# Kernel optimization log

Hardware: AMD Instinct MI355X
Metric: run time of the kernel (lower is better)

Reference implementation:

```python
import jax, jax.numpy as jnp
import numpy as np

DIM = 96
D_STATE = 16
D_CONV = 3
D_INNER = 192   # int(DIM * 2.0)
DT_RANK = 6     # ceil(DIM / 16)
K = 4           # cross-scan directions
BATCH, H, W = 2, 56, 56


def setup_inputs() -> dict:
    key = jax.random.key(0)
    k = jax.random.split(key, 8)
    x = jax.random.normal(k[0], (BATCH, DIM, H, W), jnp.float32)
    W_in = jax.random.normal(k[1], (DIM, 2 * D_INNER), jnp.float32) / np.sqrt(DIM)
    W_conv = jax.random.normal(k[2], (D_INNER, 1, D_CONV, D_CONV), jnp.float32) / D_CONV
    b_conv = jnp.zeros((D_INNER,), jnp.float32)
    W_xproj = jax.random.normal(k[3], (K, D_INNER, DT_RANK + 2 * D_STATE), jnp.float32) / np.sqrt(D_INNER)
    W_dt = jax.random.normal(k[4], (K, DT_RANK, D_INNER), jnp.float32) / np.sqrt(DT_RANK)
    # dt bias init as in torch: dt ~ exp(U * (log 0.1 - log 0.001) + log 0.001), inv-softplus
    dt = jnp.exp(jax.random.uniform(k[5], (K, D_INNER), jnp.float32)
                 * (np.log(0.1) - np.log(0.001)) + np.log(0.001))
    dt = jnp.clip(dt, 1e-4, None)
    b_dt = dt + jnp.log(-jnp.expm1(-dt))
    A_logs = jnp.log(jnp.broadcast_to(jnp.arange(1, D_STATE + 1, dtype=jnp.float32),
                                      (K, D_INNER, D_STATE)))
    Ds = jnp.ones((K, D_INNER), jnp.float32)
    W_out = jax.random.normal(k[6], (D_INNER, DIM), jnp.float32) / np.sqrt(D_INNER)
    return dict(x=x, W_in=W_in, W_conv=W_conv, b_conv=b_conv, W_xproj=W_xproj,
                W_dt=W_dt, b_dt=b_dt, A_logs=A_logs, Ds=Ds, W_out=W_out)


def _ss2d(x, W_in, W_conv, b_conv, W_xproj, W_dt, b_dt, A_logs, Ds, W_out):
    Bsz, C, Hh, Ww = x.shape
    L = Hh * Ww
    # in_proj
    xf = x.transpose(0, 2, 3, 1).reshape(Bsz, L, C)        # (B, L, C)
    xz = xf @ W_in
    xp, z = jnp.split(xz, 2, axis=-1)                       # each (B, L, D)
    # depthwise conv + silu
    xi = xp.reshape(Bsz, Hh, Ww, -1).transpose(0, 3, 1, 2)  # (B, D, H, W)
    pad = D_CONV // 2
    xi = jax.lax.conv_general_dilated(
        xi, W_conv, (1, 1), ((pad, pad), (pad, pad)),
        feature_group_count=xi.shape[1],
        dimension_numbers=('NCHW', 'OIHW', 'NCHW')) + b_conv[None, :, None, None]
    xi = jax.nn.silu(xi)
    D = xi.shape[1]
    # cross-scan: 4 directions, each (B, L, D)
    x1 = xi.reshape(Bsz, D, L).transpose(0, 2, 1)
    x2 = xi[:, :, :, ::-1].reshape(Bsz, D, L).transpose(0, 2, 1)
    xt = xi.transpose(0, 1, 3, 2)                           # (B, D, W, H)
    x3 = xt.reshape(Bsz, D, L).transpose(0, 2, 1)
    x4 = xt[:, :, :, ::-1].reshape(Bsz, D, L).transpose(0, 2, 1)
    xs = jnp.stack([x1, x2, x3, x4])                        # (K, B, L, D)
    # per-direction projections, batched over K
    xdbl = jnp.einsum('kbld,kde->kble', xs, W_xproj)
    dr = xdbl[..., :DT_RANK]
    Bk = xdbl[..., DT_RANK:DT_RANK + D_STATE]               # (K, B, L, N)
    Ck = xdbl[..., DT_RANK + D_STATE:]                      # (K, B, L, N)
    delta = jax.nn.softplus(jnp.einsum('kblr,krd->kbld', dr, W_dt)
                            + b_dt[:, None, None, :])       # (K, B, L, D)
    A = -jnp.exp(A_logs)                                    # (K, D, N)

    def step(h, inp):
        x_i, d_i, B_i, C_i = inp  # (K,B,D), (K,B,D), (K,B,N), (K,B,N)
        dA = jnp.exp(d_i[..., None] * A[:, None])           # (K, B, D, N)
        h = dA * h + (d_i * x_i)[..., None] * B_i[:, :, None, :]
        y = jnp.einsum('kbdn,kbn->kbd', h, C_i)
        return h, y

    h0 = jnp.zeros((K, Bsz, D, D_STATE), xs.dtype)
    seq = (xs.transpose(2, 0, 1, 3), delta.transpose(2, 0, 1, 3),
           Bk.transpose(2, 0, 1, 3), Ck.transpose(2, 0, 1, 3))
    _, ys = jax.lax.scan(step, h0, seq)                     # (L, K, B, D)
    ys = ys.transpose(1, 2, 0, 3) + xs * Ds[:, None, None, :]  # (K, B, L, D)
    # cross-merge back to row-major (h w) order
    y1 = ys[0]
    y2 = ys[1].reshape(Bsz, Hh, Ww, D)[:, :, ::-1, :].reshape(Bsz, L, D)
    y3 = ys[2].reshape(Bsz, Ww, Hh, D).transpose(0, 2, 1, 3).reshape(Bsz, L, D)
    y4 = ys[3].reshape(Bsz, Ww, Hh, D)[:, :, ::-1, :].transpose(0, 2, 1, 3).reshape(Bsz, L, D)
    y = (y1 + y2 + y3 + y4) * jax.nn.silu(z)
    out = (y @ W_out).reshape(Bsz, Hh, Ww, C).transpose(0, 3, 1, 2)
    return out


def reference(x, W_in, W_conv, b_conv, W_xproj, W_dt, b_dt, A_logs, Ds, W_out):
    return _ss2d(x, W_in, W_conv, b_conv, W_xproj, W_dt, b_dt, A_logs, Ds, W_out)
```

## Files before the change

kernel.cpp:

```cpp
#include <hip/hip_runtime.h>
#include <math.h>

constexpr int BATCH  = 2;
constexpr int CDIM   = 96;
constexpr int HH     = 56;
constexpr int WW     = 56;
constexpr int LL     = HH * WW;
constexpr int DIN    = 192;
constexpr int NK     = 4;
constexpr int NST    = 16;
constexpr int RNK    = 6;
constexpr int EPROJ  = RNK + 2 * NST;
constexpr int SCH    = 64;
constexpr int NCH    = LL / SCH;
constexpr int CGRP   = DIN / 16;

constexpr int STDU = SCH + 2;
constexpr int STBC = SCH + 6;
constexpr int STY  = SCH + 4;
constexpr int STB1 = SCH + 4;

constexpr size_t SZ_PX   = (size_t)BATCH * LL * DIN;
constexpr size_t OFF_XP  = 0;
constexpr size_t OFF_Z   = OFF_XP + SZ_PX;
constexpr size_t OFF_XI  = OFF_Z  + SZ_PX;
constexpr size_t OFF_DR  = OFF_XI + SZ_PX;
constexpr size_t SZ_DR   = (size_t)NK * BATCH * LL * 8;
constexpr size_t OFF_B   = OFF_DR + SZ_DR;
constexpr size_t SZ_BC   = (size_t)NK * BATCH * LL * NST;
constexpr size_t OFF_C   = OFF_B + SZ_BC;
constexpr size_t OFF_YD  = OFF_C + SZ_BC;
constexpr size_t SZ_YD   = (size_t)NK * BATCH * LL * DIN;
constexpr size_t OFF_HE  = OFF_YD + SZ_YD;
constexpr size_t SZ_HS   = (size_t)NK * BATCH * NCH * DIN * NST;
constexpr size_t OFF_HI  = OFF_HE + SZ_HS;
constexpr size_t OFF_WT  = OFF_HI + SZ_HS;
constexpr size_t SZ_WT   = (size_t)NK * EPROJ * DIN;

__device__ __forceinline__ float silu(float v) {
    return v / (1.0f + __expf(-v));
}

__device__ __forceinline__ float softplus_f(float x) {
    return (x > 20.0f) ? x : __logf(1.0f + __expf(x));
}

__device__ __forceinline__ float row_reduce16(float p) {
    p += __int_as_float(__builtin_amdgcn_update_dpp(0, __float_as_int(p), 0x128, 0xf, 0xf, true));
    p += __int_as_float(__builtin_amdgcn_update_dpp(0, __float_as_int(p), 0x124, 0xf, 0xf, true));
    p += __int_as_float(__builtin_amdgcn_update_dpp(0, __float_as_int(p), 0x122, 0xf, 0xf, true));
    p += __int_as_float(__builtin_amdgcn_update_dpp(0, __float_as_int(p), 0x121, 0xf, 0xf, true));
    return p;
}

__device__ __forceinline__ int seq_to_lr(int k, int l) {
    int q = l / WW;
    int r = l - q * WW;
    if (k == 0) return l;
    if (k == 1) return q * WW + (WW - 1 - r);
    if (k == 2) return r * WW + q;
    return (WW - 1 - r) * WW + q;
}

__device__ __forceinline__ int spatial_to_seq(int k, int s) {
    int h = s / WW;
    int w = s - h * WW;
    if (k == 0) return s;
    if (k == 1) return h * WW + (WW - 1 - w);
    if (k == 2) return w * WW + h;
    return w * WW + (WW - 1 - h);
}

__device__ __forceinline__ size_t hs_idx(int c, int kb, int d, int n) {
    return ((size_t)(c * (NK * BATCH) + kb) * DIN + d) * NST + n;
}

__device__ __forceinline__ float4 delta4(
        float4 r03, float2 r45, const float4* wr, float4 bb4) {
    float4 raw = bb4;
    raw.x = fmaf(r03.x, wr[0].x, raw.x); raw.y = fmaf(r03.x, wr[0].y, raw.y);
    raw.z = fmaf(r03.x, wr[0].z, raw.z); raw.w = fmaf(r03.x, wr[0].w, raw.w);
    raw.x = fmaf(r03.y, wr[1].x, raw.x); raw.y = fmaf(r03.y, wr[1].y, raw.y);
    raw.z = fmaf(r03.y, wr[1].z, raw.z); raw.w = fmaf(r03.y, wr[1].w, raw.w);
    raw.x = fmaf(r03.z, wr[2].x, raw.x); raw.y = fmaf(r03.z, wr[2].y, raw.y);
    raw.z = fmaf(r03.z, wr[2].z, raw.z); raw.w = fmaf(r03.z, wr[2].w, raw.w);
    raw.x = fmaf(r03.w, wr[3].x, raw.x); raw.y = fmaf(r03.w, wr[3].y, raw.y);
    raw.z = fmaf(r03.w, wr[3].z, raw.z); raw.w = fmaf(r03.w, wr[3].w, raw.w);
    raw.x = fmaf(r45.x, wr[4].x, raw.x); raw.y = fmaf(r45.x, wr[4].y, raw.y);
    raw.z = fmaf(r45.x, wr[4].z, raw.z); raw.w = fmaf(r45.x, wr[4].w, raw.w);
    raw.x = fmaf(r45.y, wr[5].x, raw.x); raw.y = fmaf(r45.y, wr[5].y, raw.y);
    raw.z = fmaf(r45.y, wr[5].z, raw.z); raw.w = fmaf(r45.y, wr[5].w, raw.w);
    raw.x = softplus_f(raw.x); raw.y = softplus_f(raw.y);
    raw.z = softplus_f(raw.z); raw.w = softplus_f(raw.w);
    return raw;
}

constexpr int K1_PIX = 8;
__global__ __launch_bounds__(384) void k_inproj(
        const float* __restrict__ x, const float* __restrict__ W_in,
        const float* __restrict__ W_xproj,
        float* __restrict__ xp, float* __restrict__ z, float* __restrict__ Wt) {
    __shared__ float sxT[CDIM][K1_PIX];
    int gp0 = blockIdx.x * K1_PIX;
    int t   = threadIdx.x;
    int b   = gp0 / LL;
    int l0  = gp0 - b * LL;
    int gid = blockIdx.x * 384 + t;
    if (gid < NK * DIN * EPROJ) {
        int k = gid / (DIN * EPROJ);
        int r = gid % (DIN * EPROJ);
        int d = r / EPROJ;
        int e = r % EPROJ;
        Wt[((size_t)k * EPROJ + e) * DIN + d] = W_xproj[gid];
    }
    for (int i = t; i < CDIM * K1_PIX; i += 384) {
        int c = i >> 3, p = i & 7;
        sxT[c][p] = x[((size_t)(b * CDIM + c)) * LL + l0 + p];
    }
    __syncthreads();
    int e = t;
    float acc[K1_PIX];
#pragma unroll
    for (int p = 0; p < K1_PIX; p++) acc[p] = 0.0f;
    const float4* sx4 = (const float4*)sxT;
#pragma unroll 4
    for (int c = 0; c < CDIM; c++) {
        float w  = W_in[c * (2 * DIN) + e];
        float4 va = sx4[2 * c];
        float4 vb = sx4[2 * c + 1];
        acc[0] = fmaf(va.x, w, acc[0]); acc[1] = fmaf(va.y, w, acc[1]);
        acc[2] = fmaf(va.z, w, acc[2]); acc[3] = fmaf(va.w, w, acc[3]);
        acc[4] = fmaf(vb.x, w, acc[4]); acc[5] = fmaf(vb.y, w, acc[5]);
        acc[6] = fmaf(vb.z, w, acc[6]); acc[7] = fmaf(vb.w, w, acc[7]);
    }
    if (e < DIN) {
#pragma unroll
        for (int p = 0; p < K1_PIX; p++)
            xp[((size_t)(gp0 + p)) * DIN + e] = acc[p];
    } else {
        int e2 = e - DIN;
#pragma unroll
        for (int p = 0; p < K1_PIX; p++)
            z[((size_t)(gp0 + p)) * DIN + e2] = acc[p];
    }
}

__global__ __launch_bounds__(192) void k_conv(
        const float* __restrict__ xp, const float* __restrict__ Wc,
        const float* __restrict__ bc, float* __restrict__ xi) {
    int gp = blockIdx.x;
    int d  = threadIdx.x;
    int b  = gp / LL;
    int l  = gp - b * LL;
    int h  = l / WW;
    int w  = l - h * WW;
    float acc = bc[d];
#pragma unroll
    for (int dy = -1; dy <= 1; dy++) {
        int hh = h + dy;
        if (hh < 0 || hh >= HH) continue;
#pragma unroll
        for (int dx = -1; dx <= 1; dx++) {
            int ww = w + dx;
            if (ww < 0 || ww >= WW) continue;
            acc = fmaf(xp[((size_t)b * LL + hh * WW + ww) * DIN + d],
                       Wc[d * 9 + (dy + 1) * 3 + (dx + 1)], acc);
        }
    }
    xi[(size_t)gp * DIN + d] = silu(acc);
}

constexpr int K3_PIX = 32;
__global__ __launch_bounds__(256) void k_xproj(
        const float* __restrict__ xi, const float* __restrict__ Wt,
        float* __restrict__ drbuf, float* __restrict__ Bbuf,
        float* __restrict__ Cbuf) {
    __shared__ float4 v4[K3_PIX][49];
    __shared__ float4 sw4[EPROJ][49];
    int k   = blockIdx.y;
    int gp0 = blockIdx.x * K3_PIX;
    int b   = gp0 / LL;
    int l0  = gp0 - b * LL;
    int t   = threadIdx.x;
    const float4* xin4 = (const float4*)(xi + (size_t)gp0 * DIN);
    for (int i = t; i < K3_PIX * 48; i += 256)
        v4[i / 48][i % 48] = xin4[i];
    const float4* wt4 = (const float4*)(Wt + (size_t)k * EPROJ * DIN);
    for (int i = t; i < EPROJ * 48; i += 256)
        sw4[i / 48][i % 48] = wt4[i];
    __syncthreads();
    int p0 = t & 15;
    int eg = t >> 4;
    bool has3 = (eg < EPROJ - 32);
    float acc[2][3] = {{0.f, 0.f, 0.f}, {0.f, 0.f, 0.f}};
    for (int j = 0; j < 48; j++) {
        float4 w0 = sw4[eg][j];
        float4 w1 = sw4[eg + 16][j];
        float4 w2 = has3 ? sw4[eg + 32][j] : make_float4(0.f, 0.f, 0.f, 0.f);
#pragma unroll
        for (int q = 0; q < 2; q++) {
            float4 vv = v4[p0 + 16 * q][j];
            acc[q][0] = fmaf(vv.x, w0.x, acc[q][0]); acc[q][0] = fmaf(vv.y, w0.y, acc[q][0]);
            acc[q][0] = fmaf(vv.z, w0.z, acc[q][0]); acc[q][0] = fmaf(vv.w, w0.w, acc[q][0]);
            acc[q][1] = fmaf(vv.x, w1.x, acc[q][1]); acc[q][1] = fmaf(vv.y, w1.y, acc[q][1]);
            acc[q][1] = fmaf(vv.z, w1.z, acc[q][1]); acc[q][1] = fmaf(vv.w, w1.w, acc[q][1]);
            acc[q][2] = fmaf(vv.x, w2.x, acc[q][2]); acc[q][2] = fmaf(vv.y, w2.y, acc[q][2]);
            acc[q][2] = fmaf(vv.z, w2.z, acc[q][2]); acc[q][2] = fmaf(vv.w, w2.w, acc[q][2]);
        }
    }
#pragma unroll
    for (int q = 0; q < 2; q++) {
        int p  = p0 + 16 * q;
        int ls = spatial_to_seq(k, l0 + p);
        size_t kb  = (size_t)(k * BATCH + b);
        size_t b8  = (kb * LL + ls) * 8;
        size_t b16 = (kb * LL + ls) * NST;
        if (eg < RNK) drbuf[b8 + eg] = acc[q][0];
        else          Bbuf[b16 + eg - RNK] = acc[q][0];
        int e1 = eg + 16;
        if (e1 < RNK + NST) Bbuf[b16 + e1 - RNK] = acc[q][1];
        else                Cbuf[b16 + e1 - RNK - NST] = acc[q][1];
        if (has3) Cbuf[b16 + eg + 32 - RNK - NST] = acc[q][2];
    }
}

__global__ __launch_bounds__(256) void k_scanA(
        const float* __restrict__ xi, const float* __restrict__ drbuf,
        const float* __restrict__ Bbuf, const float* __restrict__ A_logs,
        const float* __restrict__ W_dt, const float* __restrict__ b_dt,
        float* __restrict__ Pbuf, float* __restrict__ hend) {
    __shared__ float2 sDU2[16][STDU];
    __shared__ float  sB1t[16][STB1];
    int c   = blockIdx.x;
    int blk = blockIdx.y;
    int k   = blk / (BATCH * CGRP);
    int rem = blk % (BATCH * CGRP);
    int b   = rem / CGRP;
    int cg  = rem % CGRP;
    int d0  = cg * 16;
    int t    = threadIdx.x;
    int lane = t & 63, wave = t >> 6;
    int grp  = lane >> 4, n = lane & 15;
    int ch   = wave * 4 + grp;
    int d    = d0 + ch;
    float A = -__expf(A_logs[((size_t)(k * DIN + d)) * NST + n]);
    size_t kb = (size_t)(k * BATCH + b);
    const float* drp = drbuf + kb * LL * 8;
    const float* bp  = Bbuf  + kb * LL * NST;
    const float* up  = xi    + (size_t)b * LL * DIN;
    int ss  = t >> 2;
    int cc0 = (t & 3) * 4;
    float4 wr[RNK];
#pragma unroll
    for (int r = 0; r < RNK; r++)
        wr[r] = *(const float4*)(W_dt + ((size_t)k * RNK + r) * DIN + d0 + cc0);
    float4 bb4 = *(const float4*)(b_dt + k * DIN + d0 + cc0);
    int l0 = c * SCH;
    {
        int l  = l0 + ss;
        int lr = seq_to_lr(k, l);
        float4 r03 = *(const float4*)(drp + (size_t)l * 8);
        float2 r45 = *(const float2*)(drp + (size_t)l * 8 + 4);
        float4 dlt = delta4(r03, r45, wr, bb4);
        float4 u4  = *(const float4*)(up + (size_t)lr * DIN + d0 + cc0);
        float4 B4  = *(const float4*)(bp + (size_t)l * NST + cc0);
        sDU2[cc0 + 0][ss] = make_float2(dlt.x, dlt.x * u4.x);
        sDU2[cc0 + 1][ss] = make_float2(dlt.y, dlt.y * u4.y);
        sDU2[cc0 + 2][ss] = make_float2(dlt.z, dlt.z * u4.z);
        sDU2[cc0 + 3][ss] = make_float2(dlt.w, dlt.w * u4.w);
        sB1t[cc0 + 0][ss] = B4.x;
        sB1t[cc0 + 1][ss] = B4.y;
        sB1t[cc0 + 2][ss] = B4.z;
        sB1t[cc0 + 3][ss] = B4.w;
    }
    __syncthreads();
    float h = 0.0f, P = 1.0f;
#pragma unroll 2
    for (int s4 = 0; s4 < SCH; s4 += 4) {
        float4 duA = *(const float4*)&sDU2[ch][s4];
        float4 duB = *(const float4*)&sDU2[ch][s4 + 2];
        float4 bq  = *(const float4*)&sB1t[n][s4];
        float dA;
        dA = __expf(duA.x * A); h = fmaf(dA, h, duA.y * bq.x); P *= dA;
        dA = __expf(duA.z * A); h = fmaf(dA, h, duA.w * bq.y); P *= dA;
        dA = __expf(duB.x * A); h = fmaf(dA, h, duB.y * bq.z); P *= dA;
        dA = __expf(duB.z * A); h = fmaf(dA, h, duB.w * bq.w); P *= dA;
    }
    size_t idx = hs_idx(c, (int)kb, d, n);
    Pbuf[idx] = P;
    hend[idx] = h;
}

__global__ __launch_bounds__(256) void k_scanB(
        const float* __restrict__ Pbuf, const float* __restrict__ hend,
        float* __restrict__ hin) {
    int tid = blockIdx.x * 256 + threadIdx.x;
    int kb  = tid / (DIN * NST);
    int dn  = tid % (DIN * NST);
    float h = 0.0f;
    for (int c = 0; c < NCH; c++) {
        size_t idx = ((size_t)(c * (NK * BATCH) + kb)) * (DIN * NST) + dn;
        hin[idx] = h;
        h = fmaf(Pbuf[idx], h, hend[idx]);
    }
}

__global__ __launch_bounds__(256) void k_scanC(
        const float* __restrict__ xi, const float* __restrict__ drbuf,
        const float* __restrict__ Bbuf, const float* __restrict__ Cbuf,
        const float* __restrict__ A_logs, const float* __restrict__ W_dt,
        const float* __restrict__ b_dt, const float* __restrict__ hin,
        float* __restrict__ ydir) {
    __shared__ float2 sDU2[16][STDU];
    __shared__ float2 sBC2[16][STBC];
    __shared__ float  sY[16][STY];
    int c   = blockIdx.x;
    int blk = blockIdx.y;
    int k   = blk / (BATCH * CGRP);
    int rem = blk % (BATCH * CGRP);
    int b   = rem / CGRP;
    int cg  = rem % CGRP;
    int d0  = cg * 16;
    int t    = threadIdx.x;
    int lane = t & 63, wave = t >> 6;
    int grp  = lane >> 4, n = lane & 15;
    int ch   = wave * 4 + grp;
    int d    = d0 + ch;
    float A = -__expf(A_logs[((size_t)(k * DIN + d)) * NST + n]);
    size_t kb = (size_t)(k * BATCH + b);
    const float* drp = drbuf + kb * LL * 8;
    const float* bp  = Bbuf  + kb * LL * NST;
    const float* cp  = Cbuf  + kb * LL * NST;
    const float* up  = xi    + (size_t)b * LL * DIN;
    float*       yp  = ydir  + kb * LL * DIN;
    int ss  = t >> 2;
    int cc0 = (t & 3) * 4;
    float4 wr[RNK];
#pragma unroll
    for (int r = 0; r < RNK; r++)
        wr[r] = *(const float4*)(W_dt + ((size_t)k * RNK + r) * DIN + d0 + cc0);
    float4 bb4 = *(const float4*)(b_dt + k * DIN + d0 + cc0);
    int l0 = c * SCH;
    {
        int l  = l0 + ss;
        int lr = seq_to_lr(k, l);
        float4 r03 = *(const float4*)(drp + (size_t)l * 8);
        float2 r45 = *(const float2*)(drp + (size_t)l * 8 + 4);
        float4 dlt = delta4(r03, r45, wr, bb4);
        float4 u4  = *(const float4*)(up + (size_t)lr * DIN + d0 + cc0);
        float4 B4  = *(const float4*)(bp + (size_t)l * NST + cc0);
        float4 C4  = *(const float4*)(cp + (size_t)l * NST + cc0);
        sDU2[cc0 + 0][ss] = make_float2(dlt.x, dlt.x * u4.x);
        sDU2[cc0 + 1][ss] = make_float2(dlt.y, dlt.y * u4.y);
        sDU2[cc0 + 2][ss] = make_float2(dlt.z, dlt.z * u4.z);
        sDU2[cc0 + 3][ss] = make_float2(dlt.w, dlt.w * u4.w);
        sBC2[cc0 + 0][ss] = make_float2(B4.x, C4.x);
        sBC2[cc0 + 1][ss] = make_float2(B4.y, C4.y);
        sBC2[cc0 + 2][ss] = make_float2(B4.z, C4.z);
        sBC2[cc0 + 3][ss] = make_float2(B4.w, C4.w);
    }
    float h = hin[hs_idx(c, (int)kb, d, n)];
    __syncthreads();
#pragma unroll 2
    for (int s4 = 0; s4 < SCH; s4 += 4) {
        float4 duA = *(const float4*)&sDU2[ch][s4];
        float4 duB = *(const float4*)&sDU2[ch][s4 + 2];
        float4 bcA = *(const float4*)&sBC2[n][s4];
        float4 bcB = *(const float4*)&sBC2[n][s4 + 2];
        float dA, y0, y1, y2, y3;
        dA = __expf(duA.x * A); h = fmaf(dA, h, duA.y * bcA.x); y0 = row_reduce16(h * bcA.y);
        dA = __expf(duA.z * A); h = fmaf(dA, h, duA.w * bcA.z); y1 = row_reduce16(h * bcA.w);
        dA = __expf(duB.x * A); h = fmaf(dA, h, duB.y * bcB.x); y2 = row_reduce16(h * bcB.y);
        dA = __expf(duB.z * A); h = fmaf(dA, h, duB.w * bcB.z); y3 = row_reduce16(h * bcB.w);
        if (n == 0) *(float4*)&sY[ch][s4] = make_float4(y0, y1, y2, y3);
    }
    __syncthreads();
    for (int i = t; i < SCH * 16; i += 256) {
        int s = i >> 4, cc = i & 15;
        int lr = seq_to_lr(k, l0 + s);
        yp[(size_t)lr * DIN + d0 + cc] = sY[cc][s];
    }
}

constexpr int K5_PIX = 8;
__global__ __launch_bounds__(192) void k_out(
        const float* __restrict__ ydir, const float* __restrict__ xi,
        const float* __restrict__ zbuf, const float* __restrict__ Ds,
        const float* __restrict__ W_out, float* __restrict__ out) {
    __shared__ float g[DIN][12];
    __shared__ float so[CDIM][9];
    int gp0 = blockIdx.x * K5_PIX;
    int b   = gp0 / LL;
    int l0  = gp0 - b * LL;
    int t   = threadIdx.x;
    for (int i = t; i < K5_PIX * DIN; i += 192) {
        int p = i / DIN, dd = i % DIN;
        size_t off = (size_t)(gp0 + p) * DIN + dd;
        float y = ydir[off] + ydir[SZ_PX + off]
                + ydir[2 * SZ_PX + off] + ydir[3 * SZ_PX + off];
        float dsum = Ds[dd] + Ds[DIN + dd] + Ds[2 * DIN + dd] + Ds[3 * DIN + dd];
        y = fmaf(xi[off], dsum, y);
        g[dd][p] = y * silu(zbuf[off]);
    }
    __syncthreads();
    int f    = t % CDIM;
    int half = t / CDIM;
    float acc[4] = {0.f, 0.f, 0.f, 0.f};
#pragma unroll 4
    for (int dd = 0; dd < DIN; dd++) {
        float wv = W_out[dd * CDIM + f];
        float4 gv = *(const float4*)&g[dd][half * 4];
        acc[0] = fmaf(gv.x, wv, acc[0]);
        acc[1] = fmaf(gv.y, wv, acc[1]);
        acc[2] = fmaf(gv.z, wv, acc[2]);
        acc[3] = fmaf(gv.w, wv, acc[3]);
    }
#pragma unroll
    for (int p = 0; p < 4; p++) so[f][half * 4 + p] = acc[p];
    __syncthreads();
    for (int i = t; i < CDIM * K5_PIX; i += 192) {
        int f2 = i / K5_PIX, p2 = i % K5_PIX;
        out[((size_t)(b * CDIM + f2)) * LL + l0 + p2] = so[f2][p2];
    }
}

extern "C" void kernel_launch(void* const* d_in, const int* in_sizes, int n_in,
                              void* d_out, int out_size, void* d_ws, size_t ws_size,
                              hipStream_t stream) {
    const float* x       = (const float*)d_in[0];
    const float* W_in    = (const float*)d_in[1];
    const float* W_conv  = (const float*)d_in[2];
    const float* b_conv  = (const float*)d_in[3];
    const float* W_xproj = (const float*)d_in[4];
    const float* W_dt    = (const float*)d_in[5];
    const float* b_dt    = (const float*)d_in[6];
    const float* A_logs  = (const float*)d_in[7];
    const float* Ds      = (const float*)d_in[8];
    const float* W_out   = (const float*)d_in[9];
    float* out = (float*)d_out;
    float* ws  = (float*)d_ws;

    float* xp    = ws + OFF_XP;
    float* z     = ws + OFF_Z;
    float* xi    = ws + OFF_XI;
    float* drbuf = ws + OFF_DR;
    float* Bbuf  = ws + OFF_B;
    float* Cbuf  = ws + OFF_C;
    float* ydir  = ws + OFF_YD;
    float* hend  = ws + OFF_HE;
    float* hin   = ws + OFF_HI;
    float* Wt    = ws + OFF_WT;
    float* Pbuf  = xp;

    k_inproj<<<(BATCH * LL) / K1_PIX, 384, 0, stream>>>(x, W_in, W_xproj, xp, z, Wt);
    k_conv<<<BATCH * LL, DIN, 0, stream>>>(xp, W_conv, b_conv, xi);
    dim3 g3((BATCH * LL) / K3_PIX, NK);
    k_xproj<<<g3, 256, 0, stream>>>(xi, Wt, drbuf, Bbuf, Cbuf);
    dim3 gs(NCH, NK * BATCH * CGRP);
    k_scanA<<<gs, 256, 0, stream>>>(xi, drbuf, Bbuf, A_logs, W_dt, b_dt, Pbuf, hend);
    k_scanB<<<(NK * BATCH * DIN * NST) / 256, 256, 0, stream>>>(Pbuf, hend, hin);
    k_scanC<<<gs, 256, 0, stream>>>(xi, drbuf, Bbuf, Cbuf, A_logs, W_dt, b_dt, hin, ydir);
    k_out<<<(BATCH * LL) / K5_PIX, 192, 0, stream>>>(ydir, xi, z, Ds, W_out, out);
}
```

Measured before the change: 207.6 us.

## Materialize transposed xi copy so column-major scan directions read contiguously

The conv kernel now also writes a width-major (transposed) copy of the activated input. Directions 2 and 3 read this copy in the x-projection and scan kernels, so their per-sequence-step input loads become row-contiguous instead of strided by a full image row. Their outputs stay in transposed order and are un-transposed in the output kernel's gather. This trades an extra strided store in conv and extra workspace for coalesced reads in the scan passes.

```diff
diff --git a/kernel.cpp b/kernel.cpp
--- a/kernel.cpp
+++ b/kernel.cpp
@@ -24,7 +24,8 @@
 constexpr size_t OFF_XP  = 0;
 constexpr size_t OFF_Z   = OFF_XP + SZ_PX;
 constexpr size_t OFF_XI  = OFF_Z  + SZ_PX;
-constexpr size_t OFF_DR  = OFF_XI + SZ_PX;
+constexpr size_t OFF_XIT = OFF_XI + SZ_PX;
+constexpr size_t OFF_DR  = OFF_XIT + SZ_PX;
 constexpr size_t SZ_DR   = (size_t)NK * BATCH * LL * 8;
 constexpr size_t OFF_B   = OFF_DR + SZ_DR;
 constexpr size_t SZ_BC   = (size_t)NK * BATCH * LL * NST;
@@ -35,7 +36,6 @@
 constexpr size_t SZ_HS   = (size_t)NK * BATCH * NCH * DIN * NST;
 constexpr size_t OFF_HI  = OFF_HE + SZ_HS;
 constexpr size_t OFF_WT  = OFF_HI + SZ_HS;
-constexpr size_t SZ_WT   = (size_t)NK * EPROJ * DIN;
 
 __device__ __forceinline__ float silu(float v) {
     return v / (1.0f + __expf(-v));
@@ -43,6 +43,11 @@
 
 __device__ __forceinline__ float softplus_f(float x) {
     return (x > 20.0f) ? x : __logf(1.0f + __expf(x));
+}
+
+__device__ __forceinline__ int rev56(int l) {
+    int r = l % WW;
+    return l + 55 - 2 * r;
 }
 
 __device__ __forceinline__ float row_reduce16(float p) {
@@ -51,24 +56,6 @@
     p += __int_as_float(__builtin_amdgcn_update_dpp(0, __float_as_int(p), 0x122, 0xf, 0xf, true));
     p += __int_as_float(__builtin_amdgcn_update_dpp(0, __float_as_int(p), 0x121, 0xf, 0xf, true));
     return p;
-}
-
-__device__ __forceinline__ int seq_to_lr(int k, int l) {
-    int q = l / WW;
-    int r = l - q * WW;
-    if (k == 0) return l;
-    if (k == 1) return q * WW + (WW - 1 - r);
-    if (k == 2) return r * WW + q;
-    return (WW - 1 - r) * WW + q;
-}
-
-__device__ __forceinline__ int spatial_to_seq(int k, int s) {
-    int h = s / WW;
-    int w = s - h * WW;
-    if (k == 0) return s;
-    if (k == 1) return h * WW + (WW - 1 - w);
-    if (k == 2) return w * WW + h;
-    return w * WW + (WW - 1 - h);
 }
 
 __device__ __forceinline__ size_t hs_idx(int c, int kb, int d, int n) {
@@ -147,7 +134,8 @@
 
 __global__ __launch_bounds__(192) void k_conv(
         const float* __restrict__ xp, const float* __restrict__ Wc,
-        const float* __restrict__ bc, float* __restrict__ xi) {
+        const float* __restrict__ bc, float* __restrict__ xi,
+        float* __restrict__ xiT) {
     int gp = blockIdx.x;
     int d  = threadIdx.x;
     int b  = gp / LL;
@@ -167,12 +155,16 @@
                        Wc[d * 9 + (dy + 1) * 3 + (dx + 1)], acc);
         }
     }
-    xi[(size_t)gp * DIN + d] = silu(acc);
+    float v = silu(acc);
+    xi [(size_t)gp * DIN + d] = v;
+    int m = w * HH + h;
+    xiT[((size_t)b * LL + m) * DIN + d] = v;
 }
 
 constexpr int K3_PIX = 32;
 __global__ __launch_bounds__(256) void k_xproj(
-        const float* __restrict__ xi, const float* __restrict__ Wt,
+        const float* __restrict__ xi, const float* __restrict__ xiT,
+        const float* __restrict__ Wt,
         float* __restrict__ drbuf, float* __restrict__ Bbuf,
         float* __restrict__ Cbuf) {
     __shared__ float4 v4[K3_PIX][49];
@@ -182,7 +174,8 @@
     int b   = gp0 / LL;
     int l0  = gp0 - b * LL;
     int t   = threadIdx.x;
-    const float4* xin4 = (const float4*)(xi + (size_t)gp0 * DIN);
+    const float* src = (k >= 2) ? xiT : xi;
+    const float4* xin4 = (const float4*)(src + (size_t)gp0 * DIN);
     for (int i = t; i < K3_PIX * 48; i += 256)
         v4[i / 48][i % 48] = xin4[i];
     const float4* wt4 = (const float4*)(Wt + (size_t)k * EPROJ * DIN);
@@ -210,8 +203,8 @@
     }
 #pragma unroll
     for (int q = 0; q < 2; q++) {
-        int p  = p0 + 16 * q;
-        int ls = spatial_to_seq(k, l0 + p);
+        int m  = l0 + p0 + 16 * q;
+        int ls = (k & 1) ? rev56(m) : m;
         size_t kb  = (size_t)(k * BATCH + b);
         size_t b8  = (kb * LL + ls) * 8;
         size_t b16 = (kb * LL + ls) * NST;
@@ -225,7 +218,8 @@
 }
 
 __global__ __launch_bounds__(256) void k_scanA(
-        const float* __restrict__ xi, const float* __restrict__ drbuf,
+        const float* __restrict__ xi, const float* __restrict__ xiT,
+        const float* __restrict__ drbuf,
         const float* __restrict__ Bbuf, const float* __restrict__ A_logs,
         const float* __restrict__ W_dt, const float* __restrict__ b_dt,
         float* __restrict__ Pbuf, float* __restrict__ hend) {
@@ -247,7 +241,7 @@
     size_t kb = (size_t)(k * BATCH + b);
     const float* drp = drbuf + kb * LL * 8;
     const float* bp  = Bbuf  + kb * LL * NST;
-    const float* up  = xi    + (size_t)b * LL * DIN;
+    const float* ub  = ((k >= 2) ? xiT : xi) + (size_t)b * LL * DIN;
     int ss  = t >> 2;
     int cc0 = (t & 3) * 4;
     float4 wr[RNK];
@@ -257,12 +251,12 @@
     float4 bb4 = *(const float4*)(b_dt + k * DIN + d0 + cc0);
     int l0 = c * SCH;
     {
-        int l  = l0 + ss;
-        int lr = seq_to_lr(k, l);
+        int l    = l0 + ss;
+        int ridx = (k & 1) ? rev56(l) : l;
         float4 r03 = *(const float4*)(drp + (size_t)l * 8);
         float2 r45 = *(const float2*)(drp + (size_t)l * 8 + 4);
         float4 dlt = delta4(r03, r45, wr, bb4);
-        float4 u4  = *(const float4*)(up + (size_t)lr * DIN + d0 + cc0);
+        float4 u4  = *(const float4*)(ub + (size_t)ridx * DIN + d0 + cc0);
         float4 B4  = *(const float4*)(bp + (size_t)l * NST + cc0);
         sDU2[cc0 + 0][ss] = make_float2(dlt.x, dlt.x * u4.x);
         sDU2[cc0 + 1][ss] = make_float2(dlt.y, dlt.y * u4.y);
@@ -306,7 +300,8 @@
 }
 
 __global__ __launch_bounds__(256) void k_scanC(
-        const float* __restrict__ xi, const float* __restrict__ drbuf,
+        const float* __restrict__ xi, const float* __restrict__ xiT,
+        const float* __restrict__ drbuf,
         const float* __restrict__ Bbuf, const float* __restrict__ Cbuf,
         const float* __restrict__ A_logs, const float* __restrict__ W_dt,
         const float* __restrict__ b_dt, const float* __restrict__ hin,
@@ -331,7 +326,7 @@
     const float* drp = drbuf + kb * LL * 8;
     const float* bp  = Bbuf  + kb * LL * NST;
     const float* cp  = Cbuf  + kb * LL * NST;
-    const float* up  = xi    + (size_t)b * LL * DIN;
+    const float* ub  = ((k >= 2) ? xiT : xi) + (size_t)b * LL * DIN;
     float*       yp  = ydir  + kb * LL * DIN;
     int ss  = t >> 2;
     int cc0 = (t & 3) * 4;
@@ -342,12 +337,12 @@
     float4 bb4 = *(const float4*)(b_dt + k * DIN + d0 + cc0);
     int l0 = c * SCH;
     {
-        int l  = l0 + ss;
-        int lr = seq_to_lr(k, l);
+        int l    = l0 + ss;
+        int ridx = (k & 1) ? rev56(l) : l;
         float4 r03 = *(const float4*)(drp + (size_t)l * 8);
         float2 r45 = *(const float2*)(drp + (size_t)l * 8 + 4);
         float4 dlt = delta4(r03, r45, wr, bb4);
-        float4 u4  = *(const float4*)(up + (size_t)lr * DIN + d0 + cc0);
+        float4 u4  = *(const float4*)(ub + (size_t)ridx * DIN + d0 + cc0);
         float4 B4  = *(const float4*)(bp + (size_t)l * NST + cc0);
         float4 C4  = *(const float4*)(cp + (size_t)l * NST + cc0);
         sDU2[cc0 + 0][ss] = make_float2(dlt.x, dlt.x * u4.x);
@@ -377,8 +372,9 @@
     __syncthreads();
     for (int i = t; i < SCH * 16; i += 256) {
         int s = i >> 4, cc = i & 15;
-        int lr = seq_to_lr(k, l0 + s);
-        yp[(size_t)lr * DIN + d0 + cc] = sY[cc][s];
+        int l = l0 + s;
+        int sidx = (k & 1) ? rev56(l) : l;
+        yp[(size_t)sidx * DIN + d0 + cc] = sY[cc][s];
     }
 }
 
@@ -395,12 +391,16 @@
     int t   = threadIdx.x;
     for (int i = t; i < K5_PIX * DIN; i += 192) {
         int p = i / DIN, dd = i % DIN;
-        size_t off = (size_t)(gp0 + p) * DIN + dd;
-        float y = ydir[off] + ydir[SZ_PX + off]
-                + ydir[2 * SZ_PX + off] + ydir[3 * SZ_PX + off];
+        int l = l0 + p;
+        int h = l / WW, w = l - h * WW;
+        int m = w * HH + h;
+        size_t offL = ((size_t)b * LL + l) * DIN + dd;
+        size_t offM = ((size_t)b * LL + m) * DIN + dd;
+        float y = ydir[offL] + ydir[SZ_PX + offL]
+                + ydir[2 * SZ_PX + offM] + ydir[3 * SZ_PX + offM];
         float dsum = Ds[dd] + Ds[DIN + dd] + Ds[2 * DIN + dd] + Ds[3 * DIN + dd];
-        y = fmaf(xi[off], dsum, y);
-        g[dd][p] = y * silu(zbuf[off]);
+        y = fmaf(xi[offL], dsum, y);
+        g[dd][p] = y * silu(zbuf[offL]);
     }
     __syncthreads();
     int f    = t % CDIM;
@@ -443,6 +443,7 @@
     float* xp    = ws + OFF_XP;
     float* z     = ws + OFF_Z;
     float* xi    = ws + OFF_XI;
+    float* xiT   = ws + OFF_XIT;
     float* drbuf = ws + OFF_DR;
     float* Bbuf  = ws + OFF_B;
     float* Cbuf  = ws + OFF_C;
@@ -453,12 +454,12 @@
     float* Pbuf  = xp;
 
     k_inproj<<<(BATCH * LL) / K1_PIX, 384, 0, stream>>>(x, W_in, W_xproj, xp, z, Wt);
-    k_conv<<<BATCH * LL, DIN, 0, stream>>>(xp, W_conv, b_conv, xi);
+    k_conv<<<BATCH * LL, DIN, 0, stream>>>(xp, W_conv, b_conv, xi, xiT);
     dim3 g3((BATCH * LL) / K3_PIX, NK);
-    k_xproj<<<g3, 256, 0, stream>>>(xi, Wt, drbuf, Bbuf, Cbuf);
+    k_xproj<<<g3, 256, 0, stream>>>(xi, xiT, Wt, drbuf, Bbuf, Cbuf);
     dim3 gs(NCH, NK * BATCH * CGRP);
-    k_scanA<<<gs, 256, 0, stream>>>(xi, drbuf, Bbuf, A_logs, W_dt, b_dt, Pbuf, hend);
+    k_scanA<<<gs, 256, 0, stream>>>(xi, xiT, drbuf, Bbuf, A_logs, W_dt, b_dt, Pbuf, hend);
     k_scanB<<<(NK * BATCH * DIN * NST) / 256, 256, 0, stream>>>(Pbuf, hend, hin);
-    k_scanC<<<gs, 256, 0, stream>>>(xi, drbuf, Bbuf, Cbuf, A_logs, W_dt, b_dt, hin, ydir);
+    k_scanC<<<gs, 256, 0, stream>>>(xi, xiT, drbuf, Bbuf, Cbuf, A_logs, W_dt, b_dt, hin, ydir);
     k_out<<<(BATCH * LL) / K5_PIX, 192, 0, stream>>>(ydir, xi, z, Ds, W_out, out);
 }
```

After: 210.7 us. No clear change (+1.5%).
